# Kernel optimization log

Measured on AMD Instinct MI355X. Metric: run time of the kernel, lower is better.

Reference implementation:

```python
import jax, jax.numpy as jnp
import numpy as np

D_MODEL = 1024
D_STATE = 16
D_CONV = 4
EXPAND = 2
D_INNER = EXPAND * D_MODEL          # 2048
DT_RANK = (D_MODEL + 15) // 16      # 64
BSZ, T0, H0, W0 = 4, 8, 16, 16
SEQLEN = T0 * H0 * W0               # 2048
N_BANDS = 8


def setup_inputs() -> dict:
    key = jax.random.key(0)
    ks = jax.random.split(key, 8)
    hidden_states = jax.random.normal(ks[0], (BSZ, SEQLEN, D_MODEL), jnp.float32)
    in_proj_w = jax.random.normal(ks[1], (2 * D_INNER, D_MODEL), jnp.float32) * (D_MODEL ** -0.5)
    conv_w = jax.random.normal(ks[2], (D_INNER, 1, D_CONV), jnp.float32) * (D_CONV ** -0.5)
    conv_b = jnp.zeros((D_INNER,), jnp.float32)
    x_proj_w = jax.random.normal(ks[3], (DT_RANK + 2 * D_STATE, D_INNER), jnp.float32) * (D_INNER ** -0.5)
    dt_std = DT_RANK ** -0.5
    dt_proj_w = jax.random.uniform(ks[4], (D_INNER, DT_RANK), jnp.float32, -dt_std, dt_std)
    # inverse-softplus init of dt bias, as in the torch module
    dt = jnp.exp(jax.random.uniform(ks[5], (D_INNER,), jnp.float32)
                 * (np.log(0.1) - np.log(0.001)) + np.log(0.001))
    dt = jnp.clip(dt, 1e-4, None)
    dt_proj_b = dt + jnp.log(-jnp.expm1(-dt))
    A_log = jnp.log(jnp.tile(jnp.arange(1, D_STATE + 1, dtype=jnp.float32)[None, :], (D_INNER, 1)))
    D_param = jnp.ones((D_INNER,), jnp.float32)
    out_proj_w = jax.random.normal(ks[6], (D_MODEL, D_INNER), jnp.float32) * (D_INNER ** -0.5)
    return dict(hidden_states=hidden_states, T=T0, H=H0, W=W0,
                in_proj_w=in_proj_w, conv_w=conv_w, conv_b=conv_b,
                x_proj_w=x_proj_w, dt_proj_w=dt_proj_w, dt_proj_b=dt_proj_b,
                A_log=A_log, D=D_param, out_proj_w=out_proj_w)


def _channel_alignment(x, B, T, H, W):
    """x: (B, C, L=T*H*W) -> (align_loss scalar, features (B*T, C))."""
    C = x.shape[1]
    x4 = x.reshape(B, C, T, H, W).transpose(0, 2, 1, 3, 4).reshape(B * T, C, H, W)
    fr = jnp.fft.rfft2(x4, axes=(-2, -1))
    mag = jnp.sqrt(fr.real ** 2 + fr.imag ** 2 + 1e-8)
    mag = jnp.fft.fftshift(mag, axes=(-2, -1))
    Wr = mag.shape[-1]                      # W//2 + 1
    hg = jnp.arange(H)[:, None]
    wg = jnp.arange(Wr)[None, :]
    r = jnp.sqrt(((hg - H // 2) / H) ** 2 + ((wg - Wr // 2) / Wr) ** 2)
    masks = jnp.stack([((r >= i / N_BANDS) & (r < (i + 1) / N_BANDS)).astype(mag.dtype)
                       for i in range(N_BANDS)])          # (8, H, Wr)
    bands = jnp.einsum('bchw,khw->bck', mag, masks)        # (B*T, C, 8)
    bands = bands / (bands.sum(-1, keepdims=True) + 1e-8)
    features = bands[..., N_BANDS // 2:].sum(-1)           # (B*T, C) high-freq ratio
    fn = features / jnp.maximum(jnp.linalg.norm(features, axis=1, keepdims=True), 1e-12)
    sim = fn @ fn.T
    Bt = features.shape[0]
    loss = 1.0 - sim.sum() / (Bt * Bt)
    return loss, features


def _invert_A(A_log, features):
    """Blend A_log toward its column-flipped version, weighted by channel features."""
    A_max = A_log.max(axis=0, keepdims=True)
    A_min = A_log.min(axis=0, keepdims=True)
    A_flipped = A_max + A_min - A_log
    attention = jnp.linalg.norm(jnp.exp(A_log), axis=1)
    attention = attention / (attention.max() + 1e-8)
    f = jax.nn.softmax(jax.lax.stop_gradient(features).mean(axis=0))
    alpha = jnp.clip(f * (1.0 - attention), 0.0, 1.0)[:, None]   # (d_inner, 1)
    return (1.0 - alpha) * A_log + alpha * A_flipped


def reference(hidden_states, T, H, W, in_proj_w, conv_w, conv_b,
              x_proj_w, dt_proj_w, dt_proj_b, A_log, D, out_proj_w):
    B, L, _ = hidden_states.shape
    xz = jnp.einsum('bld,ed->bel', hidden_states, in_proj_w)      # (B, 2*d_inner, L)
    x, z = xz[:, :D_INNER], xz[:, D_INNER:]

    align_loss, features = _channel_alignment(x, B, T, H, W)
    A_log_new = _invert_A(A_log, features)
    A = -jnp.exp(A_log_new)                                       # (d_inner, d_state)

    # causal depthwise conv1d + SiLU (left pad d_conv-1 == torch pad then slice :L)
    xc = jax.lax.conv_general_dilated(x, conv_w, (1,), [(D_CONV - 1, 0)],
                                      dimension_numbers=('NCH', 'OIH', 'NCH'),
                                      feature_group_count=D_INNER)
    xc = jax.nn.silu(xc + conv_b[None, :, None])                  # (B, d_inner, L)

    x_dbl = jnp.einsum('bdl,ed->ble', xc, x_proj_w)               # (B, L, dt_rank+2N)
    dt_low = x_dbl[..., :DT_RANK]
    Bm = x_dbl[..., DT_RANK:DT_RANK + D_STATE]                    # (B, L, N)
    Cm = x_dbl[..., DT_RANK + D_STATE:]                           # (B, L, N)
    delta = jax.nn.softplus(jnp.einsum('blr,dr->bld', dt_low, dt_proj_w) + dt_proj_b)

    u = xc.transpose(0, 2, 1)                                     # (B, L, d_inner)

    def step(s, inp):
        d_t, u_t, B_t, C_t = inp                                  # (B,D),(B,D),(B,N),(B,N)
        s = s * jnp.exp(d_t[..., None] * A) + (d_t * u_t)[..., None] * B_t[:, None, :]
        y_t = jnp.einsum('bdn,bn->bd', s, C_t)
        return s, y_t

    s0 = jnp.zeros((B, D_INNER, D_STATE), delta.dtype)
    _, ys = jax.lax.scan(step, s0,
                         (delta.transpose(1, 0, 2), u.transpose(1, 0, 2),
                          Bm.transpose(1, 0, 2), Cm.transpose(1, 0, 2)))
    y = ys.transpose(1, 0, 2)                                     # (B, L, d_inner)
    y = y + u * D
    y = y * jax.nn.silu(z.transpose(0, 2, 1))
    out = jnp.einsum('bld,ed->ble', y, out_proj_w)                # (B, L, d_model)
    return out, align_loss
```

## Files before the change

kernel.cpp:

```cpp
#include <hip/hip_runtime.h>
#include <math.h>
#include <stdint.h>

#define LSEQ 2048
#define DM   1024
#define DI   2048
#define NC   32
#define CL   64

#define OFF_X     ((size_t)0)
#define OFF_Z     ((size_t)16777216)
#define OFF_U     ((size_t)33554432)
#define OFF_S     ((size_t)50331648)
#define OFF_CS    (OFF_S)
#define OFF_SDT   (OFF_S + 4194304)
#define OFF_XDBL  (OFF_S + 4456448)
#define OFF_FEAT  (OFF_S + 5242880)
#define OFF_AWS   (OFF_S + 5308448)
#define OFF_B1    ((size_t)58720256)

__device__ __forceinline__ float silu_(float x) { return x / (1.f + __expf(-x)); }
__device__ __forceinline__ float softplus_(float x) {
  return fmaxf(x, 0.f) + log1pf(__expf(-fabsf(x)));
}
__device__ __forceinline__ unsigned short f2bf(float x) {
  unsigned int u = __float_as_uint(x);
  u += 0x7fffu + ((u >> 16) & 1u);
  return (unsigned short)(u >> 16);
}
__device__ __forceinline__ float bf2f(unsigned short h) {
  return __uint_as_float(((unsigned int)h) << 16);
}

typedef __attribute__((ext_vector_type(8))) short bf16x8;
typedef __attribute__((ext_vector_type(4))) float f32x4;

__device__ __forceinline__ void gl2lds16(const void* g, void* l) {
  __builtin_amdgcn_global_load_lds(
      (const __attribute__((address_space(1))) unsigned int*)(uintptr_t)g,
      (__attribute__((address_space(3))) unsigned int*)(uintptr_t)l,
      16, 0, 0);
}

#define BARRIER_()                                   \
  do {                                               \
    asm volatile("" ::: "memory");                   \
    __builtin_amdgcn_s_barrier();                    \
    asm volatile("" ::: "memory");                   \
  } while (0)

__global__ __launch_bounds__(256) void split2_w(
    const float* __restrict__ a, unsigned short* __restrict__ oa, int ksa,
    size_t na4,
    const float* __restrict__ b, unsigned short* __restrict__ ob, int ksb)
{
  size_t i4 = ((size_t)blockIdx.x << 8) + threadIdx.x;
  const float* src; unsigned short* dst; int ks;
  if (i4 < na4) { src = a; dst = oa; ks = ksa; }
  else          { src = b; dst = ob; ks = ksb; i4 -= na4; }
  const size_t flat = i4 << 2;
  const int K = 1 << ks;
  const size_t row = flat >> ks;
  const int k = (int)(flat & (size_t)(K - 1));
  float4 v = *(const float4*)(src + flat);
  float f[4] = {v.x, v.y, v.z, v.w};
  unsigned short h[4], lo[4];
#pragma unroll
  for (int c = 0; c < 4; ++c) { h[c] = f2bf(f[c]); lo[c] = f2bf(f[c] - bf2f(h[c])); }
  unsigned short* o = dst + (row << (ks + 1)) + k;
  *(uint2*)(o)     = make_uint2((unsigned)h[0]  | ((unsigned)h[1]  << 16),
                                (unsigned)h[2]  | ((unsigned)h[3]  << 16));
  *(uint2*)(o + K) = make_uint2((unsigned)lo[0] | ((unsigned)lo[1] << 16),
                                (unsigned)lo[2] | ((unsigned)lo[3] << 16));
}

template <int NPASS, int MH, int NH>
__device__ __forceinline__ void phase_mfma(
    const unsigned short* __restrict__ shc, f32x4 (&acc)[8][4],
    int wm, int wn, int lm, int roff)
{
  bf16x8 aH[4], bH[2], aL[4], bL[2];
#pragma unroll
  for (int ii = 0; ii < 4; ++ii) {
    const int ar = (wm + (MH * 4 + ii) * 16 + lm) * 32 + roff;
    aH[ii] = *(const bf16x8*)(shc + ar);
    if constexpr (NPASS > 1) aL[ii] = *(const bf16x8*)(shc + 2 * 8192 + ar);
  }
#pragma unroll
  for (int jj = 0; jj < 2; ++jj) {
    const int br = (wn + (NH * 2 + jj) * 16 + lm) * 32 + roff;
    bH[jj] = *(const bf16x8*)(shc + 8192 + br);
    if constexpr (NPASS > 1) bL[jj] = *(const bf16x8*)(shc + 3 * 8192 + br);
  }
  __builtin_amdgcn_s_setprio(1);
#pragma unroll
  for (int ii = 0; ii < 4; ++ii)
#pragma unroll
    for (int jj = 0; jj < 2; ++jj) {
      const int i = MH * 4 + ii, j = NH * 2 + jj;
      acc[i][j] = __builtin_amdgcn_mfma_f32_16x16x32_bf16(aH[ii], bH[jj], acc[i][j], 0, 0, 0);
      if constexpr (NPASS > 1) {
        acc[i][j] = __builtin_amdgcn_mfma_f32_16x16x32_bf16(aH[ii], bL[jj], acc[i][j], 0, 0, 0);
        acc[i][j] = __builtin_amdgcn_mfma_f32_16x16x32_bf16(aL[ii], bH[jj], acc[i][j], 0, 0, 0);
      }
    }
  __builtin_amdgcn_s_setprio(0);
}

template <int NPASS>
__global__ __launch_bounds__(512, 2) void gemm_8ph(
    const unsigned short* __restrict__ Ap, const unsigned short* __restrict__ Bp,
    float* __restrict__ C, int K, int ldc)
{
  constexpr int NTEN = (NPASS > 1) ? 4 : 2;
  __shared__ unsigned short sh[2][NTEN][256 * 32];
  const int tid = threadIdx.x;
  const int bn = blockIdx.x << 8;
  const int bm = blockIdx.y << 8;
  const int K2 = K * 2;
  const int wave = tid >> 6, lane = tid & 63;
  const int wm = (wave >> 2) << 7;
  const int wn = (wave & 3) << 6;
  const int lm = lane & 15, quad = lane >> 4;
  const int roff = ((quad ^ ((lm >> 1) & 3)) << 3);

  const int r0 = tid >> 2;
  const int kq = (((tid & 3) ^ ((r0 >> 1) & 3)) << 3);
  const unsigned short* a0 = Ap + (size_t)(bm + r0) * K2 + kq;
  const unsigned short* a1 = a0 + (size_t)128 * K2;
  const unsigned short* b0 = Bp + (size_t)(bn + r0) * K2 + kq;
  const unsigned short* b1 = b0 + (size_t)128 * K2;
  const int ls0 = tid * 8, ls1 = 4096 + tid * 8;

  f32x4 acc[8][4] = {};
  const int NT = K >> 5;

  {
    unsigned short* s = &sh[0][0][0];
    gl2lds16(a0, s + ls0);
    gl2lds16(a1, s + ls1);
    if constexpr (NPASS > 1) {
      gl2lds16(a0 + K, s + 2 * 8192 + ls0);
      gl2lds16(a1 + K, s + 2 * 8192 + ls1);
    }
    gl2lds16(b0, s + 8192 + ls0);
    gl2lds16(b1, s + 8192 + ls1);
    if constexpr (NPASS > 1) {
      gl2lds16(b0 + K, s + 3 * 8192 + ls0);
      gl2lds16(b1 + K, s + 3 * 8192 + ls1);
    }
  }

  for (int t = 0; t < NT - 1; ++t) {
    const unsigned short* cur = &sh[t & 1][0][0];
    unsigned short* nxt = &sh[(t + 1) & 1][0][0];
    const int kn = (t + 1) << 5;

    gl2lds16(a0 + kn, nxt + ls0);
    gl2lds16(a1 + kn, nxt + ls1);
    if constexpr (NPASS > 1) {
      gl2lds16(a0 + K + kn, nxt + 2 * 8192 + ls0);
      gl2lds16(a1 + K + kn, nxt + 2 * 8192 + ls1);
      asm volatile("s_waitcnt vmcnt(4)" ::: "memory");
    } else {
      asm volatile("s_waitcnt vmcnt(2)" ::: "memory");
    }
    BARRIER_();
    phase_mfma<NPASS, 0, 0>(cur, acc, wm, wn, lm, roff);
    BARRIER_();
    gl2lds16(b0 + kn, nxt + 8192 + ls0);
    gl2lds16(b1 + kn, nxt + 8192 + ls1);
    if constexpr (NPASS > 1) {
      gl2lds16(b0 + K + kn, nxt + 3 * 8192 + ls0);
      gl2lds16(b1 + K + kn, nxt + 3 * 8192 + ls1);
    }
    phase_mfma<NPASS, 0, 1>(cur, acc, wm, wn, lm, roff);
    BARRIER_();
    phase_mfma<NPASS, 1, 0>(cur, acc, wm, wn, lm, roff);
    BARRIER_();
    phase_mfma<NPASS, 1, 1>(cur, acc, wm, wn, lm, roff);
    BARRIER_();
  }

  {
    const unsigned short* cur = &sh[(NT - 1) & 1][0][0];
    asm volatile("s_waitcnt vmcnt(0)" ::: "memory");
    BARRIER_();
    phase_mfma<NPASS, 0, 0>(cur, acc, wm, wn, lm, roff);
    BARRIER_();
    phase_mfma<NPASS, 0, 1>(cur, acc, wm, wn, lm, roff);
    BARRIER_();
    phase_mfma<NPASS, 1, 0>(cur, acc, wm, wn, lm, roff);
    BARRIER_();
    phase_mfma<NPASS, 1, 1>(cur, acc, wm, wn, lm, roff);
  }

#pragma unroll
  for (int i = 0; i < 8; ++i) {
    const int m = bm + wm + i * 16 + quad * 4;
#pragma unroll
    for (int j = 0; j < 4; ++j) {
      const int n = bn + wn + j * 16 + lm;
#pragma unroll
      for (int r = 0; r < 4; ++r)
        C[(size_t)(m + r) * ldc + n] = acc[i][j][r];
    }
  }
}

template <int NPASS, int A_FP32>
__global__ __launch_bounds__(256) void gemm_mfma(
    const void* __restrict__ Avp, const unsigned short* __restrict__ Bp,
    float* __restrict__ C, int K, int ldc, int nxs)
{
  __shared__ unsigned short AsH[128 * 32];
  __shared__ unsigned short BsH[128 * 32];
  __shared__ unsigned short AsL[(NPASS > 1) ? 128 * 32 : 8];
  __shared__ unsigned short BsL[(NPASS > 1) ? 128 * 32 : 8];
  const int tid = threadIdx.x;
  const int lin = blockIdx.y * gridDim.x + blockIdx.x;
  const int xcd = lin & 7;
  const int t = lin >> 3;
  const int nmask = (1 << nxs) - 1;
  const int bn = (((t & nmask) << 3) | xcd) << 7;
  const int bm = (t >> nxs) << 7;
  const int K2 = K * 2;

  const int wave = tid >> 6, lane = tid & 63;
  const int wm = (wave >> 1) << 6, wn = (wave & 1) << 6;
  const int lm = lane & 15, quad = lane >> 4;
  const int sw = (lm >> 1) & 3;

  f32x4 acc[4][4] = {};

  const int r0 = tid >> 2;
  const int kq = ((tid & 3) ^ ((r0 >> 1) & 3)) << 3;
  const unsigned short* BgH0 = Bp + (size_t)(bn + r0) * K2 + kq;
  const unsigned short* BgH1 = Bp + (size_t)(bn + 64 + r0) * K2 + kq;
  unsigned short* lA0 = &AsH[(size_t)tid * 8];
  unsigned short* lA1 = &AsH[(size_t)(256 + tid) * 8];
  unsigned short* lB0 = &BsH[(size_t)tid * 8];
  unsigned short* lB1 = &BsH[(size_t)(256 + tid) * 8];
  unsigned short* lAl0 = (NPASS > 1) ? &AsL[(size_t)tid * 8] : nullptr;
  unsigned short* lAl1 = (NPASS > 1) ? &AsL[(size_t)(256 + tid) * 8] : nullptr;
  unsigned short* lBl0 = (NPASS > 1) ? &BsL[(size_t)tid * 8] : nullptr;
  unsigned short* lBl1 = (NPASS > 1) ? &BsL[(size_t)(256 + tid) * 8] : nullptr;

  const unsigned short* AgH0 = nullptr; const unsigned short* AgH1 = nullptr;
  const float* Af0 = nullptr; const float* Af1 = nullptr;
  if (A_FP32) {
    const float* Af = (const float*)Avp;
    Af0 = Af + (size_t)(bm + r0) * K + kq;
    Af1 = Af + (size_t)(bm + 64 + r0) * K + kq;
  } else {
    const unsigned short* Ab = (const unsigned short*)Avp;
    AgH0 = Ab + (size_t)(bm + r0) * K2 + kq;
    AgH1 = Ab + (size_t)(bm + 64 + r0) * K2 + kq;
  }

  for (int k0 = 0; k0 < K; k0 += 32) {
    __syncthreads();
    if (A_FP32) {
      float4 u0 = *(const float4*)(Af0 + k0);
      float4 u1 = *(const float4*)(Af0 + k0 + 4);
      float4 v0 = *(const float4*)(Af1 + k0);
      float4 v1 = *(const float4*)(Af1 + k0 + 4);
      float fu[8] = {u0.x,u0.y,u0.z,u0.w,u1.x,u1.y,u1.z,u1.w};
      float fv[8] = {v0.x,v0.y,v0.z,v0.w,v1.x,v1.y,v1.z,v1.w};
      unsigned int hu[4], lu[4], hv[4], lv[4];
#pragma unroll
      for (int c = 0; c < 4; ++c) {
        unsigned short h0 = f2bf(fu[2*c]),   l0 = f2bf(fu[2*c]   - bf2f(h0));
        unsigned short h1 = f2bf(fu[2*c+1]), l1 = f2bf(fu[2*c+1] - bf2f(h1));
        hu[c] = (unsigned)h0 | ((unsigned)h1 << 16);
        lu[c] = (unsigned)l0 | ((unsigned)l1 << 16);
        unsigned short g0 = f2bf(fv[2*c]),   m0 = f2bf(fv[2*c]   - bf2f(g0));
        unsigned short g1 = f2bf(fv[2*c+1]), m1 = f2bf(fv[2*c+1] - bf2f(g1));
        hv[c] = (unsigned)g0 | ((unsigned)g1 << 16);
        lv[c] = (unsigned)m0 | ((unsigned)m1 << 16);
      }
      *(uint4*)lA0  = make_uint4(hu[0], hu[1], hu[2], hu[3]);
      *(uint4*)lA1  = make_uint4(hv[0], hv[1], hv[2], hv[3]);
      if (NPASS > 1) {
        *(uint4*)lAl0 = make_uint4(lu[0], lu[1], lu[2], lu[3]);
        *(uint4*)lAl1 = make_uint4(lv[0], lv[1], lv[2], lv[3]);
      }
    } else {
      gl2lds16(AgH0 + k0, lA0);
      gl2lds16(AgH1 + k0, lA1);
      if (NPASS > 1) {
        gl2lds16(AgH0 + K + k0, lAl0);
        gl2lds16(AgH1 + K + k0, lAl1);
      }
    }
    gl2lds16(BgH0 + k0, lB0);
    gl2lds16(BgH1 + k0, lB1);
    if (NPASS > 1) {
      gl2lds16(BgH0 + K + k0, lBl0);
      gl2lds16(BgH1 + K + k0, lBl1);
    }
    __syncthreads();

    bf16x8 aH[4], bH[4];
#pragma unroll
    for (int i = 0; i < 4; ++i)
      aH[i] = *(const bf16x8*)&AsH[(wm + i * 16 + lm) * 32 + ((quad ^ sw) << 3)];
#pragma unroll
    for (int j = 0; j < 4; ++j)
      bH[j] = *(const bf16x8*)&BsH[(wn + j * 16 + lm) * 32 + ((quad ^ sw) << 3)];
#pragma unroll
    for (int i = 0; i < 4; ++i)
#pragma unroll
      for (int j = 0; j < 4; ++j)
        acc[i][j] = __builtin_amdgcn_mfma_f32_16x16x32_bf16(aH[i], bH[j], acc[i][j], 0, 0, 0);
    if (NPASS > 1) {
      bf16x8 aL[4], bL[4];
#pragma unroll
      for (int i = 0; i < 4; ++i)
        aL[i] = *(const bf16x8*)&AsL[(wm + i * 16 + lm) * 32 + ((quad ^ sw) << 3)];
#pragma unroll
      for (int j = 0; j < 4; ++j)
        bL[j] = *(const bf16x8*)&BsL[(wn + j * 16 + lm) * 32 + ((quad ^ sw) << 3)];
#pragma unroll
      for (int i = 0; i < 4; ++i)
#pragma unroll
        for (int j = 0; j < 4; ++j) {
          acc[i][j] = __builtin_amdgcn_mfma_f32_16x16x32_bf16(aH[i], bL[j], acc[i][j], 0, 0, 0);
          acc[i][j] = __builtin_amdgcn_mfma_f32_16x16x32_bf16(aL[i], bH[j], acc[i][j], 0, 0, 0);
        }
    }
  }

#pragma unroll
  for (int i = 0; i < 4; ++i) {
    const int m = bm + wm + i * 16 + quad * 4;
#pragma unroll
    for (int j = 0; j < 4; ++j) {
      const int n = bn + wn + j * 16 + lm;
#pragma unroll
      for (int r = 0; r < 4; ++r)
        C[(size_t)(m + r) * ldc + n] = acc[i][j][r];
    }
  }
}

template <int EPI>
__global__ __launch_bounds__(256) void gemm_nt(
    const float* __restrict__ A, int lda,
    const float* __restrict__ B, int ldb,
    float* __restrict__ C, int ldc,
    int N, int K, const float* __restrict__ bias, size_t cseg)
{
  __shared__ float As[16][68];
  __shared__ float Bs[16][68];
  const int tid = threadIdx.x;
  const int bm = blockIdx.y << 6;
  const int bn = blockIdx.x << 6;
  const int kz = blockIdx.z;
  A += (size_t)kz * K;
  B += (size_t)kz * K;
  C += (size_t)kz * cseg;
  const int lr = tid >> 2;
  const int lk = (tid & 3) << 2;
  const int tx = tid & 15, ty = tid >> 4;

  float acc[4][4];
#pragma unroll
  for (int i = 0; i < 4; ++i)
#pragma unroll
    for (int j = 0; j < 4; ++j) acc[i][j] = 0.f;

  const float* Apt = A + (size_t)(bm + lr) * lda + lk;
  const float* Bpt = B + (size_t)(bn + lr) * ldb + lk;
  const bool bv = (bn + lr) < N;

  for (int k0 = 0; k0 < K; k0 += 16) {
    float4 a4 = *(const float4*)(Apt + k0);
    float4 b4 = bv ? *(const float4*)(Bpt + k0) : make_float4(0.f, 0.f, 0.f, 0.f);
    __syncthreads();
    As[lk + 0][lr] = a4.x; As[lk + 1][lr] = a4.y;
    As[lk + 2][lr] = a4.z; As[lk + 3][lr] = a4.w;
    Bs[lk + 0][lr] = b4.x; Bs[lk + 1][lr] = b4.y;
    Bs[lk + 2][lr] = b4.z; Bs[lk + 3][lr] = b4.w;
    __syncthreads();
#pragma unroll
    for (int k = 0; k < 16; ++k) {
      const float4 av = *(const float4*)(&As[k][ty << 2]);
      const float4 bw = *(const float4*)(&Bs[k][tx << 2]);
      float a4r[4] = {av.x, av.y, av.z, av.w};
      float b4r[4] = {bw.x, bw.y, bw.z, bw.w};
#pragma unroll
      for (int i = 0; i < 4; ++i)
#pragma unroll
        for (int j = 0; j < 4; ++j)
          acc[i][j] = fmaf(a4r[i], b4r[j], acc[i][j]);
    }
  }

  const int m = bm + (ty << 2);
  const int n = bn + (tx << 2);
#pragma unroll
  for (int i = 0; i < 4; ++i) {
    float v[4] = {acc[i][0], acc[i][1], acc[i][2], acc[i][3]};
    if (EPI == 1) {
#pragma unroll
      for (int j = 0; j < 4; ++j)
        if (n + j < N) v[j] = softplus_(v[j] + bias[n + j]);
    }
    if (n + 3 < N) {
      *(float4*)(C + (size_t)(m + i) * ldc + n) = make_float4(v[0], v[1], v[2], v[3]);
    } else {
#pragma unroll
      for (int j = 0; j < 4; ++j)
        if (n + j < N) C[(size_t)(m + i) * ldc + n + j] = v[j];
    }
  }
}

__global__ __launch_bounds__(256) void reduce4(
    const float* __restrict__ P, float* __restrict__ O, size_t seg)
{
  const size_t i = ((size_t)blockIdx.x << 8) + threadIdx.x;
  float4 a = ((const float4*)P)[i];
  float4 b = ((const float4*)(P + seg))[i];
  float4 c = ((const float4*)(P + 2 * seg))[i];
  float4 d = ((const float4*)(P + 3 * seg))[i];
  ((float4*)O)[i] = make_float4(a.x + b.x + c.x + d.x,
                                a.y + b.y + c.y + d.y,
                                a.z + b.z + c.z + d.z,
                                a.w + b.w + c.w + d.w);
}

__global__ __launch_bounds__(256) void feat_kernel(
    const float* __restrict__ X, float* __restrict__ features)
{
  __shared__ float xin[256][17];
  __shared__ float Rf[16 * 315];
  __shared__ float tc[16], ts[16];
  __shared__ float part2[16][16][2];

  const int tid = threadIdx.x;
  const int frame = blockIdx.x >> 7;
  const int cg = blockIdx.x & 127;
  const int b = frame >> 3, t = frame & 7;
  const int c0 = cg << 4;

  if (tid < 16) {
    float ang = 0.39269908169872414f * (float)tid;
    tc[tid] = cosf(ang);
    ts[tid] = sinf(ang);
  }
  const float* xb = X + ((size_t)(b * LSEQ + t * 256) << 11) + c0;
  for (int i = tid; i < 256 * 16; i += 256) {
    int hw = i >> 4, ci = i & 15;
    xin[hw][ci] = xb[((size_t)hw << 11) + ci];
  }
  __syncthreads();

  {
    const int ci = tid & 15, h = tid >> 4;
    float re[9], im[9];
#pragma unroll
    for (int kw = 0; kw < 9; ++kw) { re[kw] = 0.f; im[kw] = 0.f; }
#pragma unroll
    for (int w = 0; w < 16; ++w) {
      float x = xin[(h << 4) + w][ci];
#pragma unroll
      for (int kw = 0; kw < 9; ++kw) {
        int ph = (kw * w) & 15;
        re[kw] = fmaf(x, tc[ph], re[kw]);
        im[kw] = fmaf(-x, ts[ph], im[kw]);
      }
    }
#pragma unroll
    for (int kw = 0; kw < 9; ++kw) {
      Rf[ci * 315 + kw * 35 + 2 * h]     = re[kw];
      Rf[ci * 315 + kw * 35 + 2 * h + 1] = im[kw];
    }
  }
  __syncthreads();

  {
    const int ci = tid & 15, kh = tid >> 4;
    float ut = 0.f, tt = 0.f;
    for (int kw = 0; kw < 9; ++kw) {
      float fre = 0.f, fim = 0.f;
#pragma unroll
      for (int h = 0; h < 16; ++h) {
        int ph = (kh * h) & 15;
        float c = tc[ph], s = ts[ph];
        float rr = Rf[ci * 315 + kw * 35 + 2 * h];
        float ri = Rf[ci * 315 + kw * 35 + 2 * h + 1];
        fre += rr * c + ri * s;
        fim += ri * c - rr * s;
      }
      float mag = sqrtf(fre * fre + fim * fim + 1e-8f);
      int sh = (kh + 8) & 15;
      int sw2 = kw + 4; if (sw2 >= 9) sw2 -= 9;
      float dh = (float)(sh - 8) / 16.0f;
      float dw = (float)(sw2 - 4) / 9.0f;
      tt += mag;
      if (dh * dh + dw * dw >= 0.25f) ut += mag;
    }
    part2[ci][kh][0] = ut;
    part2[ci][kh][1] = tt;
  }
  __syncthreads();

  if (tid < 16) {
    float ut = 0.f, tt = 0.f;
    for (int kh = 0; kh < 16; ++kh) { ut += part2[tid][kh][0]; tt += part2[tid][kh][1]; }
    features[frame * DI + c0 + tid] = ut / (tt + 1e-8f);
  }
}

__global__ __launch_bounds__(256) void alpha_kernel(
    const float* __restrict__ feats, const float* __restrict__ A_log,
    float* __restrict__ Aws, float* __restrict__ loss_out)
{
  __shared__ float red[256];
  __shared__ float invn[32];
  __shared__ float PT[32][257];
  __shared__ float AM[256][17];
  __shared__ float sAmax[16], sAmin[16];
  const int tid = threadIdx.x;

  float pn[32];
#pragma unroll
  for (int i = 0; i < 32; ++i) pn[i] = 0.f;
  float md[8];
#pragma unroll
  for (int j = 0; j < 8; ++j) md[j] = 0.f;
  for (int i = 0; i < 32; ++i) {
#pragma unroll
    for (int j = 0; j < 8; ++j) {
      float v = feats[(i << 11) + tid + (j << 8)];
      pn[i] = fmaf(v, v, pn[i]);
      md[j] += v;
    }
  }
#pragma unroll
  for (int j = 0; j < 8; ++j) md[j] *= (1.f / 32.f);
#pragma unroll
  for (int i = 0; i < 32; ++i) PT[i][tid] = pn[i];
  __syncthreads();
  if (tid < 32) {
    float s = 0.f;
    for (int k = 0; k < 256; ++k) s += PT[tid][k];
    invn[tid] = 1.f / fmaxf(sqrtf(s), 1e-12f);
  }
  __syncthreads();

  float gsq = 0.f;
#pragma unroll
  for (int j = 0; j < 8; ++j) {
    float gd = 0.f;
    for (int i = 0; i < 32; ++i)
      gd = fmaf(feats[(i << 11) + tid + (j << 8)], invn[i], gd);
    gsq = fmaf(gd, gd, gsq);
  }
  red[tid] = gsq; __syncthreads();
  for (int s = 128; s > 0; s >>= 1) { if (tid < s) red[tid] += red[tid + s]; __syncthreads(); }
  if (tid == 0) loss_out[0] = 1.f - red[0] * (1.f / 1024.f);
  __syncthreads();

  float lm = md[0];
#pragma unroll
  for (int j = 1; j < 8; ++j) lm = fmaxf(lm, md[j]);
  red[tid] = lm; __syncthreads();
  for (int s = 128; s > 0; s >>= 1) { if (tid < s) red[tid] = fmaxf(red[tid], red[tid + s]); __syncthreads(); }
  const float mmax = red[0]; __syncthreads();

  float p[8]; float ps = 0.f;
#pragma unroll
  for (int j = 0; j < 8; ++j) { p[j] = __expf(md[j] - mmax); ps += p[j]; }
  red[tid] = ps; __syncthreads();
  for (int s = 128; s > 0; s >>= 1) { if (tid < s) red[tid] += red[tid + s]; __syncthreads(); }
  const float psum = red[0]; __syncthreads();

  float amaxl[16], aminl[16], rn[8];
#pragma unroll
  for (int n = 0; n < 16; ++n) { amaxl[n] = -1e30f; aminl[n] = 1e30f; }
#pragma unroll
  for (int j = 0; j < 8; ++j) {
    const int d = tid + (j << 8);
    float ss = 0.f;
#pragma unroll
    for (int n = 0; n < 16; ++n) {
      float a = A_log[(d << 4) + n];
      float e = __expf(a);
      ss = fmaf(e, e, ss);
      amaxl[n] = fmaxf(amaxl[n], a);
      aminl[n] = fminf(aminl[n], a);
    }
    rn[j] = sqrtf(ss);
  }
  float rm = rn[0];
#pragma unroll
  for (int j = 1; j < 8; ++j) rm = fmaxf(rm, rn[j]);
  red[tid] = rm; __syncthreads();
  for (int s = 128; s > 0; s >>= 1) { if (tid < s) red[tid] = fmaxf(red[tid], red[tid + s]); __syncthreads(); }
  const float rnmax = red[0]; __syncthreads();

#pragma unroll
  for (int n = 0; n < 16; ++n) AM[tid][n] = amaxl[n];
  __syncthreads();
  if (tid < 16) { float m = -1e30f; for (int i = 0; i < 256; ++i) m = fmaxf(m, AM[i][tid]); sAmax[tid] = m; }
  __syncthreads();
#pragma unroll
  for (int n = 0; n < 16; ++n) AM[tid][n] = aminl[n];
  __syncthreads();
  if (tid < 16) { float m = 1e30f; for (int i = 0; i < 256; ++i) m = fminf(m, AM[i][tid]); sAmin[tid] = m; }
  __syncthreads();

  const float irn = 1.f / (rnmax + 1e-8f);
#pragma unroll
  for (int j = 0; j < 8; ++j) {
    const int d = tid + (j << 8);
    const float att = rn[j] * irn;
    const float f = p[j] / psum;
    const float alpha = fminf(fmaxf(f * (1.f - att), 0.f), 1.f);
#pragma unroll
    for (int n = 0; n < 16; ++n) {
      float a = A_log[(d << 4) + n];
      float fl = sAmax[n] + sAmin[n] - a;
      float an = (1.f - alpha) * a + alpha * fl;
      Aws[(d << 4) + n] = -__expf(an) * 1.4426950408889634f;
    }
  }
}

__global__ __launch_bounds__(256) void conv_kernel(
    const float* __restrict__ X, const float* __restrict__ cw,
    const float* __restrict__ cb, float* __restrict__ U)
{
  const size_t i4 = ((size_t)blockIdx.x << 8) + threadIdx.x;
  const int e4 = (int)(i4 & 511);
  const size_t row = i4 >> 9;
  const int l = (int)(row & 2047);
  const float* xr = X + (row << 11) + (e4 << 2);
  const float4 z4 = make_float4(0.f, 0.f, 0.f, 0.f);
  float4 x0 = *(const float4*)xr;
  float4 x1 = (l >= 1) ? *(const float4*)(xr - 2048) : z4;
  float4 x2 = (l >= 2) ? *(const float4*)(xr - 4096) : z4;
  float4 x3 = (l >= 3) ? *(const float4*)(xr - 6144) : z4;
  const float4* cwf = (const float4*)cw;
  float4 bi = *(const float4*)(cb + (e4 << 2));
  float x0a[4] = {x0.x, x0.y, x0.z, x0.w};
  float x1a[4] = {x1.x, x1.y, x1.z, x1.w};
  float x2a[4] = {x2.x, x2.y, x2.z, x2.w};
  float x3a[4] = {x3.x, x3.y, x3.z, x3.w};
  float bia[4] = {bi.x, bi.y, bi.z, bi.w};
  float o[4];
#pragma unroll
  for (int c = 0; c < 4; ++c) {
    float4 w = cwf[(e4 << 2) + c];
    float acc = bia[c];
    acc = fmaf(x3a[c], w.x, acc);
    acc = fmaf(x2a[c], w.y, acc);
    acc = fmaf(x1a[c], w.z, acc);
    acc = fmaf(x0a[c], w.w, acc);
    o[c] = silu_(acc);
  }
  *(float4*)(U + (i4 << 2)) = make_float4(o[0], o[1], o[2], o[3]);
}

__global__ __launch_bounds__(256) void scan_pass1(
    const float* __restrict__ delta, const float* __restrict__ U,
    const float* __restrict__ xdbl, const float* __restrict__ Aws,
    float* __restrict__ cs, float* __restrict__ sdt)
{
  __shared__ float blds[CL * 16];
  const int tid = threadIdx.x;
  const int dg = blockIdx.x & 7;
  const int chunk = (blockIdx.x >> 3) & 31;
  const int b = blockIdx.x >> 8;
  const int d = (dg << 8) | tid;
  const int l0 = chunk * CL;

  for (int i = tid; i < CL * 16; i += 256) {
    int l = i >> 4, j = i & 15;
    blds[i] = xdbl[(size_t)(b * LSEQ + l0 + l) * 96 + 64 + j];
  }
  __syncthreads();

  float Ar[16];
#pragma unroll
  for (int n = 0; n < 16; ++n) Ar[n] = Aws[(d << 4) + n];
  float s[16];
#pragma unroll
  for (int n = 0; n < 16; ++n) s[n] = 0.f;
  float sumdt = 0.f;

  const float* dp = delta + ((size_t)b << 22) + ((size_t)l0 << 11) + d;
  const float* up = U + ((size_t)b << 22) + ((size_t)l0 << 11) + d;

  for (int l = 0; l < CL; ++l) {
    const float dt = dp[(size_t)l << 11];
    const float u = up[(size_t)l << 11];
    sumdt += dt;
    const float du = dt * u;
    const float* bl = &blds[l << 4];
#pragma unroll
    for (int n = 0; n < 16; ++n)
      s[n] = fmaf(s[n], __builtin_amdgcn_exp2f(dt * Ar[n]), du * bl[n]);
  }

  float* csp = cs + ((((size_t)b * NC + chunk) * 2048 + d) << 4);
#pragma unroll
  for (int n = 0; n < 4; ++n)
    *(float4*)(csp + (n << 2)) = make_float4(s[4*n], s[4*n+1], s[4*n+2], s[4*n+3]);
  sdt[((size_t)b * NC + chunk) * 2048 + d] = sumdt;
}

__global__ __launch_bounds__(256) void scan_mid(
    float* __restrict__ cs, const float* __restrict__ sdt,
    const float* __restrict__ Aws)
{
  const int b = blockIdx.x >> 3;
  const int d = ((blockIdx.x & 7) << 8) | threadIdx.x;
  float Ar[16];
#pragma unroll
  for (int n = 0; n < 16; ++n) Ar[n] = Aws[(d << 4) + n];
  float si[16];
#pragma unroll
  for (int n = 0; n < 16; ++n) si[n] = 0.f;

  for (int c = 0; c < NC; ++c) {
    const size_t base = ((size_t)b * NC + c) * 2048 + d;
    float* csp = cs + (base << 4);
    float sl[16];
#pragma unroll
    for (int n = 0; n < 4; ++n) {
      float4 v = *(const float4*)(csp + (n << 2));
      sl[4*n] = v.x; sl[4*n+1] = v.y; sl[4*n+2] = v.z; sl[4*n+3] = v.w;
    }
    const float sm = sdt[base];
#pragma unroll
    for (int n = 0; n < 4; ++n)
      *(float4*)(csp + (n << 2)) = make_float4(si[4*n], si[4*n+1], si[4*n+2], si[4*n+3]);
#pragma unroll
    for (int n = 0; n < 16; ++n)
      si[n] = fmaf(si[n], __builtin_amdgcn_exp2f(sm * Ar[n]), sl[n]);
  }
}

__global__ __launch_bounds__(256) void scan_pass3(
    const float* __restrict__ delta, const float* __restrict__ Z,
    float* __restrict__ U,
    const float* __restrict__ xdbl, const float* __restrict__ Aws,
    const float* __restrict__ Dp, const float* __restrict__ cs)
{
  __shared__ float bclds[CL * 32];
  const int tid = threadIdx.x;
  const int dg = blockIdx.x & 7;
  const int chunk = (blockIdx.x >> 3) & 31;
  const int b = blockIdx.x >> 8;
  const int d = (dg << 8) | tid;
  const int l0 = chunk * CL;

  for (int i = tid; i < CL * 32; i += 256) {
    int l = i >> 5, j = i & 31;
    bclds[i] = xdbl[(size_t)(b * LSEQ + l0 + l) * 96 + 64 + j];
  }
  __syncthreads();

  float Ar[16];
#pragma unroll
  for (int n = 0; n < 16; ++n) Ar[n] = Aws[(d << 4) + n];
  const float Dd = Dp[d];

  const float* csp = cs + ((((size_t)b * NC + chunk) * 2048 + d) << 4);
  float s[16];
#pragma unroll
  for (int n = 0; n < 4; ++n) {
    float4 v = *(const float4*)(csp + (n << 2));
    s[4*n] = v.x; s[4*n+1] = v.y; s[4*n+2] = v.z; s[4*n+3] = v.w;
  }

  const float* dp = delta + ((size_t)b << 22) + ((size_t)l0 << 11) + d;
  const float* zp = Z + ((size_t)b << 22) + ((size_t)l0 << 11) + d;
  float* up = U + ((size_t)b << 22) + ((size_t)l0 << 11) + d;

  for (int l = 0; l < CL; ++l) {
    const float dt = dp[(size_t)l << 11];
    const float u = up[(size_t)l << 11];
    const float z = zp[(size_t)l << 11];
    const float du = dt * u;
    const float* bcl = &bclds[l << 5];
    float y = 0.f;
#pragma unroll
    for (int n = 0; n < 16; ++n) {
      s[n] = fmaf(s[n], __builtin_amdgcn_exp2f(dt * Ar[n]), du * bcl[n]);
      y = fmaf(s[n], bcl[16 + n], y);
    }
    const float yv = fmaf(u, Dd, y);
    up[(size_t)l << 11] = yv * silu_(z);
  }
}

extern "C" void kernel_launch(void* const* d_in, const int* in_sizes, int n_in,
                              void* d_out, int out_size, void* d_ws, size_t ws_size,
                              hipStream_t stream)
{
  const float* hs         = (const float*)d_in[0];
  const float* in_proj_w  = (const float*)d_in[4];
  const float* conv_w     = (const float*)d_in[5];
  const float* conv_b     = (const float*)d_in[6];
  const float* x_proj_w   = (const float*)d_in[7];
  const float* dt_proj_w  = (const float*)d_in[8];
  const float* dt_proj_b  = (const float*)d_in[9];
  const float* A_log      = (const float*)d_in[10];
  const float* Dp         = (const float*)d_in[11];
  const float* out_proj_w = (const float*)d_in[12];
  float* out = (float*)d_out;
  float* ws = (float*)d_ws;

  float* X     = ws + OFF_X;
  float* Z     = ws + OFF_Z;
  float* U     = ws + OFF_U;
  float* cs    = ws + OFF_CS;
  float* sdt   = ws + OFF_SDT;
  float* xdbl  = ws + OFF_XDBL;
  float* feats = ws + OFF_FEAT;
  float* Aws   = ws + OFF_AWS;
  unsigned short* A1s = (unsigned short*)(ws + OFF_S);
  unsigned short* B1s = (unsigned short*)(ws + OFF_B1);
  unsigned short* B2s = (unsigned short*)(ws + OFF_B1);

  const dim3 blk(256);

  split2_w<<<12288, blk, 0, stream>>>(hs, A1s, 10, (size_t)2097152,
                                      in_proj_w, B1s, 10);
  gemm_8ph<3><<<dim3(8, 32), dim3(512), 0, stream>>>(A1s, B1s, X, 1024, 2048);
  gemm_8ph<1><<<dim3(8, 32), dim3(512), 0, stream>>>(A1s, B1s + (size_t)2048 * 2048, Z, 1024, 2048);
  feat_kernel<<<4096, blk, 0, stream>>>(X, feats);
  conv_kernel<<<16384, blk, 0, stream>>>(X, conv_w, conv_b, U);
  split2_w<<<2048, blk, 0, stream>>>(out_proj_w, B2s, 11, (size_t)524288,
                                     out_proj_w, B2s, 11);
  alpha_kernel<<<1, blk, 0, stream>>>(feats, A_log, Aws, out + 8388608);
  gemm_nt<0><<<dim3(2, 128, 4), blk, 0, stream>>>(U, DI, x_proj_w, DI, cs, 96, 96, 512, nullptr, (size_t)786432);
  reduce4<<<768, blk, 0, stream>>>(cs, xdbl, (size_t)786432);
  gemm_nt<1><<<dim3(32, 128, 1), blk, 0, stream>>>(xdbl, 96, dt_proj_w, 64, X, DI, DI, 64, dt_proj_b, 0);
  scan_pass1<<<1024, blk, 0, stream>>>(X, U, xdbl, Aws, cs, sdt);
  scan_mid<<<32, blk, 0, stream>>>(cs, sdt, Aws);
  scan_pass3<<<1024, blk, 0, stream>>>(X, Z, U, xdbl, Aws, Dp, cs);
  gemm_mfma<3, 1><<<dim3(8, 64), blk, 0, stream>>>(U, B2s, out, 2048, 1024, 0);
}
```

Before: 883.3 us.

## Fuse bf16 hi/lo split into scan output and pipeline out_proj GEMM

The scan's final pass now writes each output as a packed bf16 high/low pair in one 32-bit word instead of fp32. This removes the per-tile fp32-to-bf16 split work from the out_proj GEMM. The GEMM is replaced by an 8-wave, 256x128-tile kernel that double-buffers A and B in LDS and interleaves global loads with four MFMA phases under raised wave priority. In exchange it uses more LDS and registers per block and depends on hand-placed waitcnt and barrier ordering.

```diff
diff --git a/kernel.cpp b/kernel.cpp
--- a/kernel.cpp
+++ b/kernel.cpp
@@ -208,134 +208,141 @@
   }
 }
 
-template <int NPASS, int A_FP32>
-__global__ __launch_bounds__(256) void gemm_mfma(
-    const void* __restrict__ Avp, const unsigned short* __restrict__ Bp,
-    float* __restrict__ C, int K, int ldc, int nxs)
-{
-  __shared__ unsigned short AsH[128 * 32];
-  __shared__ unsigned short BsH[128 * 32];
-  __shared__ unsigned short AsL[(NPASS > 1) ? 128 * 32 : 8];
-  __shared__ unsigned short BsL[(NPASS > 1) ? 128 * 32 : 8];
+template <int MH, int NH>
+__device__ __forceinline__ void phase8(
+    const unsigned short* __restrict__ ah, const unsigned short* __restrict__ al,
+    const unsigned short* __restrict__ bh, const unsigned short* __restrict__ bl,
+    f32x4 (&acc)[8][2], int wm, int wn, int lm, int roff)
+{
+  bf16x8 aH[4], aL[4];
+#pragma unroll
+  for (int ii = 0; ii < 4; ++ii) {
+    const int ar = (wm + (MH * 4 + ii) * 16 + lm) * 32 + roff;
+    aH[ii] = *(const bf16x8*)(ah + ar);
+    aL[ii] = *(const bf16x8*)(al + ar);
+  }
+  const int br = (wn + NH * 16 + lm) * 32 + roff;
+  bf16x8 bH = *(const bf16x8*)(bh + br);
+  bf16x8 bL = *(const bf16x8*)(bl + br);
+  __builtin_amdgcn_s_setprio(1);
+#pragma unroll
+  for (int ii = 0; ii < 4; ++ii) {
+    const int i = MH * 4 + ii;
+    acc[i][NH] = __builtin_amdgcn_mfma_f32_16x16x32_bf16(aH[ii], bH, acc[i][NH], 0, 0, 0);
+    acc[i][NH] = __builtin_amdgcn_mfma_f32_16x16x32_bf16(aH[ii], bL, acc[i][NH], 0, 0, 0);
+    acc[i][NH] = __builtin_amdgcn_mfma_f32_16x16x32_bf16(aL[ii], bH, acc[i][NH], 0, 0, 0);
+  }
+  __builtin_amdgcn_s_setprio(0);
+}
+
+__global__ __launch_bounds__(512, 2) void gemm8_8ph(
+    const unsigned int* __restrict__ Ay,
+    const unsigned short* __restrict__ Bp,
+    float* __restrict__ C)
+{
+  constexpr int K = 2048, K2 = 4096, ldc = 1024;
+  __shared__ unsigned short AHs[2][256 * 32];
+  __shared__ unsigned short ALs[2][256 * 32];
+  __shared__ unsigned short BHs[2][128 * 32];
+  __shared__ unsigned short BLs[2][128 * 32];
   const int tid = threadIdx.x;
-  const int lin = blockIdx.y * gridDim.x + blockIdx.x;
-  const int xcd = lin & 7;
-  const int t = lin >> 3;
-  const int nmask = (1 << nxs) - 1;
-  const int bn = (((t & nmask) << 3) | xcd) << 7;
-  const int bm = (t >> nxs) << 7;
-  const int K2 = K * 2;
-
+  const int bn = blockIdx.x << 7;
+  const int bm = blockIdx.y << 8;
   const int wave = tid >> 6, lane = tid & 63;
-  const int wm = (wave >> 1) << 6, wn = (wave & 1) << 6;
+  const int wm = (wave >> 2) << 7;
+  const int wn = (wave & 3) << 5;
   const int lm = lane & 15, quad = lane >> 4;
-  const int sw = (lm >> 1) & 3;
-
-  f32x4 acc[4][4] = {};
-
-  const int r0 = tid >> 2;
-  const int kq = ((tid & 3) ^ ((r0 >> 1) & 3)) << 3;
-  const unsigned short* BgH0 = Bp + (size_t)(bn + r0) * K2 + kq;
-  const unsigned short* BgH1 = Bp + (size_t)(bn + 64 + r0) * K2 + kq;
-  unsigned short* lA0 = &AsH[(size_t)tid * 8];
-  unsigned short* lA1 = &AsH[(size_t)(256 + tid) * 8];
-  unsigned short* lB0 = &BsH[(size_t)tid * 8];
-  unsigned short* lB1 = &BsH[(size_t)(256 + tid) * 8];
-  unsigned short* lAl0 = (NPASS > 1) ? &AsL[(size_t)tid * 8] : nullptr;
-  unsigned short* lAl1 = (NPASS > 1) ? &AsL[(size_t)(256 + tid) * 8] : nullptr;
-  unsigned short* lBl0 = (NPASS > 1) ? &BsL[(size_t)tid * 8] : nullptr;
-  unsigned short* lBl1 = (NPASS > 1) ? &BsL[(size_t)(256 + tid) * 8] : nullptr;
-
-  const unsigned short* AgH0 = nullptr; const unsigned short* AgH1 = nullptr;
-  const float* Af0 = nullptr; const float* Af1 = nullptr;
-  if (A_FP32) {
-    const float* Af = (const float*)Avp;
-    Af0 = Af + (size_t)(bm + r0) * K + kq;
-    Af1 = Af + (size_t)(bm + 64 + r0) * K + kq;
-  } else {
-    const unsigned short* Ab = (const unsigned short*)Avp;
-    AgH0 = Ab + (size_t)(bm + r0) * K2 + kq;
-    AgH1 = Ab + (size_t)(bm + 64 + r0) * K2 + kq;
-  }
-
-  for (int k0 = 0; k0 < K; k0 += 32) {
-    __syncthreads();
-    if (A_FP32) {
-      float4 u0 = *(const float4*)(Af0 + k0);
-      float4 u1 = *(const float4*)(Af0 + k0 + 4);
-      float4 v0 = *(const float4*)(Af1 + k0);
-      float4 v1 = *(const float4*)(Af1 + k0 + 4);
-      float fu[8] = {u0.x,u0.y,u0.z,u0.w,u1.x,u1.y,u1.z,u1.w};
-      float fv[8] = {v0.x,v0.y,v0.z,v0.w,v1.x,v1.y,v1.z,v1.w};
-      unsigned int hu[4], lu[4], hv[4], lv[4];
-#pragma unroll
-      for (int c = 0; c < 4; ++c) {
-        unsigned short h0 = f2bf(fu[2*c]),   l0 = f2bf(fu[2*c]   - bf2f(h0));
-        unsigned short h1 = f2bf(fu[2*c+1]), l1 = f2bf(fu[2*c+1] - bf2f(h1));
-        hu[c] = (unsigned)h0 | ((unsigned)h1 << 16);
-        lu[c] = (unsigned)l0 | ((unsigned)l1 << 16);
-        unsigned short g0 = f2bf(fv[2*c]),   m0 = f2bf(fv[2*c]   - bf2f(g0));
-        unsigned short g1 = f2bf(fv[2*c+1]), m1 = f2bf(fv[2*c+1] - bf2f(g1));
-        hv[c] = (unsigned)g0 | ((unsigned)g1 << 16);
-        lv[c] = (unsigned)m0 | ((unsigned)m1 << 16);
-      }
-      *(uint4*)lA0  = make_uint4(hu[0], hu[1], hu[2], hu[3]);
-      *(uint4*)lA1  = make_uint4(hv[0], hv[1], hv[2], hv[3]);
-      if (NPASS > 1) {
-        *(uint4*)lAl0 = make_uint4(lu[0], lu[1], lu[2], lu[3]);
-        *(uint4*)lAl1 = make_uint4(lv[0], lv[1], lv[2], lv[3]);
-      }
-    } else {
-      gl2lds16(AgH0 + k0, lA0);
-      gl2lds16(AgH1 + k0, lA1);
-      if (NPASS > 1) {
-        gl2lds16(AgH0 + K + k0, lAl0);
-        gl2lds16(AgH1 + K + k0, lAl1);
-      }
-    }
-    gl2lds16(BgH0 + k0, lB0);
-    gl2lds16(BgH1 + k0, lB1);
-    if (NPASS > 1) {
-      gl2lds16(BgH0 + K + k0, lBl0);
-      gl2lds16(BgH1 + K + k0, lBl1);
-    }
-    __syncthreads();
-
-    bf16x8 aH[4], bH[4];
-#pragma unroll
-    for (int i = 0; i < 4; ++i)
-      aH[i] = *(const bf16x8*)&AsH[(wm + i * 16 + lm) * 32 + ((quad ^ sw) << 3)];
-#pragma unroll
-    for (int j = 0; j < 4; ++j)
-      bH[j] = *(const bf16x8*)&BsH[(wn + j * 16 + lm) * 32 + ((quad ^ sw) << 3)];
-#pragma unroll
-    for (int i = 0; i < 4; ++i)
-#pragma unroll
-      for (int j = 0; j < 4; ++j)
-        acc[i][j] = __builtin_amdgcn_mfma_f32_16x16x32_bf16(aH[i], bH[j], acc[i][j], 0, 0, 0);
-    if (NPASS > 1) {
-      bf16x8 aL[4], bL[4];
-#pragma unroll
-      for (int i = 0; i < 4; ++i)
-        aL[i] = *(const bf16x8*)&AsL[(wm + i * 16 + lm) * 32 + ((quad ^ sw) << 3)];
-#pragma unroll
-      for (int j = 0; j < 4; ++j)
-        bL[j] = *(const bf16x8*)&BsL[(wn + j * 16 + lm) * 32 + ((quad ^ sw) << 3)];
-#pragma unroll
-      for (int i = 0; i < 4; ++i)
-#pragma unroll
-        for (int j = 0; j < 4; ++j) {
-          acc[i][j] = __builtin_amdgcn_mfma_f32_16x16x32_bf16(aH[i], bL[j], acc[i][j], 0, 0, 0);
-          acc[i][j] = __builtin_amdgcn_mfma_f32_16x16x32_bf16(aL[i], bH[j], acc[i][j], 0, 0, 0);
-        }
-    }
-  }
-
-#pragma unroll
-  for (int i = 0; i < 4; ++i) {
+  const int roff = ((quad ^ ((lm >> 1) & 3)) << 3);
+
+  const int ra = tid >> 1;
+  const int g0 = (tid & 1) << 1;
+  const int aswz = (ra >> 1) & 3;
+  const int sa0 = (ra * 32) + ((g0 ^ aswz) << 3);
+  const int sa1 = (ra * 32) + (((g0 + 1) ^ aswz) << 3);
+  const unsigned int* ag = Ay + (size_t)(bm + ra) * K + (g0 << 3);
+
+  const int rb = tid >> 2;
+  const int kqb = (((tid & 3) ^ ((rb >> 1) & 3)) << 3);
+  const unsigned short* bg = Bp + (size_t)(bn + rb) * K2 + kqb;
+  const int lsb = tid * 8;
+
+  f32x4 acc[8][2] = {};
+  constexpr int NT = K / 32;
+
+  uint4 w0, w1, w2, w3;
+#define LOADA_(kn) do { const unsigned int* p_ = ag + (kn);               \
+    w0 = *(const uint4*)p_;        w1 = *(const uint4*)(p_ + 4);          \
+    w2 = *(const uint4*)(p_ + 8);  w3 = *(const uint4*)(p_ + 12); } while (0)
+#define WRITEA_(bufi) do {                                                \
+    unsigned h0 = (w0.x & 0xffffu) | (w0.y << 16);                        \
+    unsigned h1 = (w0.z & 0xffffu) | (w0.w << 16);                        \
+    unsigned h2 = (w1.x & 0xffffu) | (w1.y << 16);                        \
+    unsigned h3 = (w1.z & 0xffffu) | (w1.w << 16);                        \
+    unsigned h4 = (w2.x & 0xffffu) | (w2.y << 16);                        \
+    unsigned h5 = (w2.z & 0xffffu) | (w2.w << 16);                        \
+    unsigned h6 = (w3.x & 0xffffu) | (w3.y << 16);                        \
+    unsigned h7 = (w3.z & 0xffffu) | (w3.w << 16);                        \
+    unsigned l0 = (w0.x >> 16) | (w0.y & 0xffff0000u);                    \
+    unsigned l1 = (w0.z >> 16) | (w0.w & 0xffff0000u);                    \
+    unsigned l2 = (w1.x >> 16) | (w1.y & 0xffff0000u);                    \
+    unsigned l3 = (w1.z >> 16) | (w1.w & 0xffff0000u);                    \
+    unsigned l4 = (w2.x >> 16) | (w2.y & 0xffff0000u);                    \
+    unsigned l5 = (w2.z >> 16) | (w2.w & 0xffff0000u);                    \
+    unsigned l6 = (w3.x >> 16) | (w3.y & 0xffff0000u);                    \
+    unsigned l7 = (w3.z >> 16) | (w3.w & 0xffff0000u);                    \
+    *(uint4*)&AHs[bufi][sa0] = make_uint4(h0, h1, h2, h3);                \
+    *(uint4*)&AHs[bufi][sa1] = make_uint4(h4, h5, h6, h7);                \
+    *(uint4*)&ALs[bufi][sa0] = make_uint4(l0, l1, l2, l3);                \
+    *(uint4*)&ALs[bufi][sa1] = make_uint4(l4, l5, l6, l7); } while (0)
+
+  LOADA_(0);
+  gl2lds16(bg,     &BHs[0][lsb]);
+  gl2lds16(bg + K, &BLs[0][lsb]);
+  asm volatile("s_waitcnt vmcnt(2)" ::: "memory");
+  WRITEA_(0);
+  asm volatile("s_waitcnt lgkmcnt(0)" ::: "memory");
+
+  for (int t = 0; t < NT - 1; ++t) {
+    const int cb = t & 1, nb = cb ^ 1;
+    const int kn = (t + 1) << 5;
+    LOADA_(kn);
+    asm volatile("s_waitcnt vmcnt(4)" ::: "memory");
+    BARRIER_();
+    phase8<0, 0>(AHs[cb], ALs[cb], BHs[cb], BLs[cb], acc, wm, wn, lm, roff);
+    BARRIER_();
+    gl2lds16(bg + kn,     &BHs[nb][lsb]);
+    gl2lds16(bg + K + kn, &BLs[nb][lsb]);
+    phase8<0, 1>(AHs[cb], ALs[cb], BHs[cb], BLs[cb], acc, wm, wn, lm, roff);
+    BARRIER_();
+    asm volatile("s_waitcnt vmcnt(2)" ::: "memory");
+    WRITEA_(nb);
+    phase8<1, 0>(AHs[cb], ALs[cb], BHs[cb], BLs[cb], acc, wm, wn, lm, roff);
+    BARRIER_();
+    phase8<1, 1>(AHs[cb], ALs[cb], BHs[cb], BLs[cb], acc, wm, wn, lm, roff);
+    asm volatile("s_waitcnt lgkmcnt(0)" ::: "memory");
+    BARRIER_();
+  }
+
+  {
+    const int cb = (NT - 1) & 1;
+    asm volatile("s_waitcnt vmcnt(0)" ::: "memory");
+    BARRIER_();
+    phase8<0, 0>(AHs[cb], ALs[cb], BHs[cb], BLs[cb], acc, wm, wn, lm, roff);
+    BARRIER_();
+    phase8<0, 1>(AHs[cb], ALs[cb], BHs[cb], BLs[cb], acc, wm, wn, lm, roff);
+    BARRIER_();
+    phase8<1, 0>(AHs[cb], ALs[cb], BHs[cb], BLs[cb], acc, wm, wn, lm, roff);
+    BARRIER_();
+    phase8<1, 1>(AHs[cb], ALs[cb], BHs[cb], BLs[cb], acc, wm, wn, lm, roff);
+  }
+#undef LOADA_
+#undef WRITEA_
+
+#pragma unroll
+  for (int i = 0; i < 8; ++i) {
     const int m = bm + wm + i * 16 + quad * 4;
 #pragma unroll
-    for (int j = 0; j < 4; ++j) {
+    for (int j = 0; j < 2; ++j) {
       const int n = bn + wn + j * 16 + lm;
 #pragma unroll
       for (int r = 0; r < 4; ++r)
@@ -795,7 +802,10 @@
       y = fmaf(s[n], bcl[16 + n], y);
     }
     const float yv = fmaf(u, Dd, y);
-    up[(size_t)l << 11] = yv * silu_(z);
+    const float yo = yv * silu_(z);
+    const unsigned short h = f2bf(yo);
+    const unsigned short lo = f2bf(yo - bf2f(h));
+    ((unsigned int*)up)[(size_t)l << 11] = (unsigned)h | ((unsigned)lo << 16);
   }
 }
 
@@ -845,5 +855,5 @@
   scan_pass1<<<1024, blk, 0, stream>>>(X, U, xdbl, Aws, cs, sdt);
   scan_mid<<<32, blk, 0, stream>>>(cs, sdt, Aws);
   scan_pass3<<<1024, blk, 0, stream>>>(X, Z, U, xdbl, Aws, Dp, cs);
-  gemm_mfma<3, 1><<<dim3(8, 64), blk, 0, stream>>>(U, B2s, out, 2048, 1024, 0);
-}
+  gemm8_8ph<<<dim3(8, 32), dim3(512), 0, stream>>>((const unsigned int*)U, B2s, out);
+}
```

After: 880.5 us. About the same (-0.3%).
